# Kernel optimization log

Hardware: AMD Instinct MI355X
Metric: run time of the kernel (lower is better)

Reference implementation:

```python
import jax, jax.numpy as jnp
import numpy as np

N_GRAPHS = 500
CHAIN = 200
D_STATE = 64
HID = 128
NEG_SLOPE = 0.2  # PyG GATConv default


def setup_inputs() -> dict:
    key = jax.random.key(0)
    ks = jax.random.split(key, 9)
    N = N_GRAPHS * CHAIN
    # batched bidirectional chain graphs (as in create_chain_graph_batch)
    off = np.arange(N_GRAPHS, dtype=np.int32) * CHAIN
    a = (off[:, None] + np.arange(CHAIN - 1, dtype=np.int32)[None, :]).ravel()
    b = a + 1
    edge_index = jnp.asarray(np.stack([np.concatenate([a, b]), np.concatenate([b, a])]), dtype=jnp.int32)
    x = jax.random.normal(ks[0], (N, D_STATE), jnp.float32)
    s1 = 1.0 / np.sqrt(D_STATE)
    W1 = jax.random.normal(ks[1], (D_STATE, 2 * HID), jnp.float32) * s1
    att_src1 = jax.random.normal(ks[2], (2, HID), jnp.float32) * (1.0 / np.sqrt(HID))
    att_dst1 = jax.random.normal(ks[3], (2, HID), jnp.float32) * (1.0 / np.sqrt(HID))
    b1 = jnp.zeros((2 * HID,), jnp.float32)
    s2 = 1.0 / np.sqrt(2 * HID)
    W2 = jax.random.normal(ks[4], (2 * HID, HID), jnp.float32) * s2
    att_src2 = jax.random.normal(ks[5], (1, HID), jnp.float32) * (1.0 / np.sqrt(HID))
    att_dst2 = jax.random.normal(ks[6], (1, HID), jnp.float32) * (1.0 / np.sqrt(HID))
    b2 = jnp.zeros((HID,), jnp.float32)
    return {"x": x, "edge_index": edge_index, "W1": W1, "att_src1": att_src1,
            "att_dst1": att_dst1, "b1": b1, "W2": W2, "att_src2": att_src2,
            "att_dst2": att_dst2, "b2": b2}


def gat_conv(x, src, dst, W, att_src, att_dst, bias, concat):
    # PyG GATConv: per-head linear, additive attention, segment softmax over dst
    N = x.shape[0]
    H, C = att_src.shape
    h = (x @ W).reshape(N, H, C)                          # [N,H,C]
    a_s = (h * att_src).sum(-1)                           # [N,H]
    a_d = (h * att_dst).sum(-1)                           # [N,H]
    logits = jax.nn.leaky_relu(a_s[src] + a_d[dst], NEG_SLOPE)  # [E,H]
    m = jax.ops.segment_max(logits, dst, num_segments=N)
    e = jnp.exp(logits - m[dst])
    s = jax.ops.segment_sum(e, dst, num_segments=N)
    alpha = e / (s[dst] + 1e-16)                          # [E,H]
    out = jax.ops.segment_sum(h[src] * alpha[:, :, None], dst, num_segments=N)  # [N,H,C]
    out = out.reshape(N, H * C) if concat else out.mean(axis=1)
    return out + bias


def reference(x, edge_index, W1, att_src1, att_dst1, b1, W2, att_src2, att_dst2, b2):
    N = x.shape[0]
    loop = jnp.arange(N, dtype=edge_index.dtype)
    src = jnp.concatenate([edge_index[0], loop])  # add_self_loops=True (PyG default)
    dst = jnp.concatenate([edge_index[1], loop])
    h = gat_conv(x, src, dst, W1, att_src1, att_dst1, b1, concat=True)
    h = jax.nn.gelu(h, approximate=False)  # torch F.gelu default = exact erf
    h = gat_conv(h, src, dst, W2, att_src2, att_dst2, b2, concat=False)
    return jax.nn.gelu(h, approximate=False)
```

## Files before the change

kernel.cpp:

```cpp
#include <hip/hip_runtime.h>
#include <hip/hip_bf16.h>

#define NG 500
#define CH 200
#define NN (NG*CH)
#define DS 64
#define HDIM 128
#define C1 256
#define NEG_SLOPE 0.2f
#define GB 1563

typedef unsigned short ushort_t;
typedef __attribute__((ext_vector_type(8))) short bf16x8;
typedef __attribute__((ext_vector_type(4))) float f32x4;

__device__ __forceinline__ float us2f(ushort_t u){
  union { unsigned int i; float f; } v; v.i = ((unsigned int)u) << 16; return v.f;
}
__device__ __forceinline__ ushort_t f2us(float f){
  union { float f; unsigned int i; } v; v.f = f;
  unsigned int x = v.i;
  return (ushort_t)((x + 0x7fffu + ((x >> 16) & 1u)) >> 16);
}
__device__ __forceinline__ unsigned int cvt_pk_bf16(float a, float b){
  unsigned int r;
  asm("v_cvt_pk_bf16_f32 %0, %1, %2" : "=v"(r) : "v"(a), "v"(b));
  return r;
}
__device__ __forceinline__ float lrelu(float v){ return v > 0.f ? v : NEG_SLOPE * v; }
__device__ __forceinline__ float gelu_fast(float x){
  float x2 = x * x;
  float zn = x * fmaf(-0.0713548163f, x2, -1.5957691216f);
  float e  = __expf(zn);
  return x * __builtin_amdgcn_rcpf(1.f + e);
}

__global__ void probe_dtype(const void* __restrict__ x, int* __restrict__ flag){
  __shared__ int cnt;
  if (threadIdx.x == 0) cnt = 0;
  __syncthreads();
  const ushort_t* p = (const ushort_t*)x;
  int local = 0;
  for (int i = threadIdx.x; i < 8192; i += 256) {
    float v = us2f(p[i]);
    if (!(fabsf(v) < 100.f)) local++;
  }
  atomicAdd(&cnt, local);
  __syncthreads();
  if (threadIdx.x == 0) flag[0] = (cnt > 16) ? 1 : 0;
}

__global__ void prep_w(const int* __restrict__ flag,
                       const void* W1, const void* as1, const void* ad1, const void* b1,
                       const void* W2, const void* as2, const void* ad2, const void* b2,
                       ushort_t* w1t, ushort_t* w2t,
                       float* asrc1f, float* adst1f, float* b1f,
                       float* asrc2f, float* adst2f, float* b2f,
                       ushort_t* wsd1, ushort_t* wsd2)
{
  const bool F = flag[0] != 0;
  int i = blockIdx.x * 256 + threadIdx.x;
  #define LD(p, j) (F ? ((const float*)(p))[j] : us2f(((const ushort_t*)(p))[j]))
  if (i < 16384)      { int k = i >> 8, n = i & 255; w1t[n*64  + k] = f2us(LD(W1, i)); }
  else if (i < 49152) { int j = i - 16384, k = j >> 7, n = j & 127; w2t[n*256 + k] = f2us(LD(W2, j)); }
  else if (i < 49408) { asrc1f[i-49152] = LD(as1, i-49152); }
  else if (i < 49664) { adst1f[i-49408] = LD(ad1, i-49408); }
  else if (i < 49920) { b1f[i-49664]    = LD(b1,  i-49664); }
  else if (i < 50048) { asrc2f[i-49920] = LD(as2, i-49920); }
  else if (i < 50176) { adst2f[i-50048] = LD(ad2, i-50048); }
  else if (i < 50304) { b2f[i-50176]    = LD(b2,  i-50176); }
  else if (i < 50560) {
    int j = i - 50304, k = j >> 2, c = j & 3;
    int head = c >> 1;
    const void* av = (c & 1) ? ad1 : as1;
    float s = 0.f;
    for (int cc = 0; cc < 128; cc++)
      s += LD(W1, k*256 + head*128 + cc) * LD(av, head*128 + cc);
    ushort_t hi = f2us(s);
    wsd1[c*64 + k] = hi;
    wsd1[(c+4)*64 + k] = f2us(s - us2f(hi));
  }
  else if (i < 51072) {
    int j = i - 50560, k = j >> 1, c = j & 1;
    const void* av = c ? ad2 : as2;
    float s = 0.f;
    for (int cc = 0; cc < 128; cc++)
      s += LD(W2, k*128 + cc) * LD(av, cc);
    ushort_t hi = f2us(s);
    wsd2[c*256 + k] = hi;
    wsd2[(c+2)*256 + k] = f2us(s - us2f(hi));
  }
  else if (i < 51584) { wsd1[512  + (i - 51072)] = 0; }
  else if (i < 54656) { wsd2[1024 + (i - 51584)] = 0; }
  #undef LD
}

__global__ __launch_bounds__(256, 4) void fused(
    const int* __restrict__ flag, const void* __restrict__ x,
    const ushort_t* __restrict__ w1t, const ushort_t* __restrict__ w2t,
    const ushort_t* __restrict__ wsd1, const ushort_t* __restrict__ wsd2,
    const float* __restrict__ b1f, const float* __restrict__ b2f,
    void* __restrict__ out)
{
  __shared__ ushort_t lds[17952];
  __shared__ float scratch[800];
  ushort_t* As  = lds;
  ushort_t* g1L = lds;

  const int t  = threadIdx.x;
  const int m0 = blockIdx.x * 64;
  const int l = t & 63, w = t >> 6;
  const int ln = l & 15, quad = l >> 4;
  const bool F = flag[0] != 0;

  #pragma unroll
  for (int i = 0; i < 5; i++) {
    int q = t + i*256;
    int r = q >> 4, off = (q & 15) * 4;
    int gr = m0 - 2 + r;
    if (r < 68 && gr >= 0 && gr < NN) {
      if (F) {
        float4 xv = *(const float4*)(&((const float*)x)[(size_t)gr*DS + off]);
        uint2 u; u.x = cvt_pk_bf16(xv.x, xv.y); u.y = cvt_pk_bf16(xv.z, xv.w);
        *(uint2*)(&As[r*72 + off]) = u;
      } else {
        *(ushort4*)(&As[r*72 + off]) = *(const ushort4*)(&((const ushort_t*)x)[(size_t)gr*DS + off]);
      }
    } else {
      ushort4 z = {0,0,0,0};
      *(ushort4*)(&As[r*72 + off]) = z;
    }
  }

  f32x4 acc[5][4];
  #pragma unroll
  for (int mi = 0; mi < 5; mi++)
    #pragma unroll
    for (int nj = 0; nj < 4; nj++) acc[mi][nj] = (f32x4){0.f,0.f,0.f,0.f};
  f32x4 acc_att[5];
  #pragma unroll
  for (int mi = 0; mi < 5; mi++) acc_att[mi] = (f32x4){0.f,0.f,0.f,0.f};

  __syncthreads();
  #pragma unroll
  for (int h = 0; h < 2; h++) {
    #pragma unroll
    for (int ks = 0; ks < 2; ks++) {
      const int kk = ks*32 + quad*8;
      bf16x8 a[5], b[2];
      #pragma unroll
      for (int njl = 0; njl < 2; njl++)
        b[njl] = *(const bf16x8*)(&w1t[(w*64 + h*32 + njl*16 + ln)*64 + kk]);
      #pragma unroll
      for (int mi = 0; mi < 5; mi++) a[mi] = *(const bf16x8*)(&As[(mi*16 + ln)*72 + kk]);
      #pragma unroll
      for (int mi = 0; mi < 5; mi++)
        #pragma unroll
        for (int njl = 0; njl < 2; njl++)
          acc[mi][2*h+njl] = __builtin_amdgcn_mfma_f32_16x16x32_bf16(a[mi], b[njl], acc[mi][2*h+njl], 0, 0, 0);
      if (h == 0 && w == 0) {
        bf16x8 batt = *(const bf16x8*)(&wsd1[ln*64 + kk]);
        #pragma unroll
        for (int mi = 0; mi < 5; mi++)
          acc_att[mi] = __builtin_amdgcn_mfma_f32_16x16x32_bf16(a[mi], batt, acc_att[mi], 0, 0, 0);
      }
    }
  }

  if (w == 0) {
    #pragma unroll
    for (int mi = 0; mi < 5; mi++)
      #pragma unroll
      for (int r = 0; r < 4; r++) {
        float v = acc_att[mi][r];
        float vc = v + __shfl(v, (l + 4) & 63, 64);
        int row = mi*16 + quad*4 + r;
        if (ln < 4 && row < 68) scratch[ln*68 + row] = vc;
      }
  }
  __syncthreads();

  if (t < 132) {
    int hh = (t >= 66) ? 1 : 0;
    int n  = t - 66*hh;
    int gj = m0 - 1 + n;
    int p  = gj % CH;
    const float* Sa = &scratch[(2*hh)*68];
    const float* Da = &scratch[(2*hh+1)*68];
    float ad = Da[n+1], as_s = Sa[n+1], as_l = Sa[n], as_r = Sa[n+2];
    bool hl = p > 0, hr = p < CH-1;
    float zs = lrelu(as_s + ad);
    float zl = hl ? lrelu(as_l + ad) : -1e30f;
    float zr = hr ? lrelu(as_r + ad) : -1e30f;
    float mx = fmaxf(zs, fmaxf(zl, zr));
    float el = hl ? __expf(zl - mx) : 0.f;
    float es = __expf(zs - mx);
    float er = hr ? __expf(zr - mx) : 0.f;
    float inv = __builtin_amdgcn_rcpf(el + es + er + 1e-16f);
    scratch[272 + n*8 + hh*4 + 0] = el*inv;
    scratch[272 + n*8 + hh*4 + 1] = es*inv;
    scratch[272 + n*8 + hh*4 + 2] = er*inv;
  }
  __syncthreads();

  {
    float b1v[4];
    #pragma unroll
    for (int nj = 0; nj < 4; nj++) b1v[nj] = b1f[w*64 + nj*16 + ln];
    if (t < 128) {
      int rr = (t < 64) ? 0 : 67;
      int c4 = (t & 63) * 4;
      ushort4 z = {0,0,0,0};
      *(ushort4*)(&g1L[rr*264 + c4]) = z;
    }
    const int head = w >> 1;
    #pragma unroll
    for (int mi = 0; mi < 5; mi++) {
      const int mip = (mi < 4) ? mi+1 : 4;
      const int mim = (mi > 0) ? mi-1 : 0;
      float hp3[4], hm0[4];
      #pragma unroll
      for (int nj = 0; nj < 4; nj++) {
        float up_a = __shfl(acc[mi ][nj][0], (l+16)&63, 64);
        float up_b = __shfl(acc[mip][nj][0], (l+16)&63, 64);
        float dn_a = __shfl(acc[mi ][nj][3], (l-16)&63, 64);
        float dn_b = __shfl(acc[mim][nj][3], (l-16)&63, 64);
        hp3[nj] = (quad < 3) ? up_a : up_b;
        hm0[nj] = (quad > 0) ? dn_a : dn_b;
      }
      #pragma unroll
      for (int r = 0; r < 4; r++) {
        int row = mi*16 + quad*4 + r;
        if (row >= 1 && row <= 66) {
          float4 av = *(const float4*)(&scratch[272 + (row-1)*8 + head*4]);
          float o[4];
          #pragma unroll
          for (int nj = 0; nj < 4; nj++) {
            float self = acc[mi][nj][r];
            float hm = (r > 0) ? acc[mi][nj][r-1] : hm0[nj];
            float hp = (r < 3) ? acc[mi][nj][r+1] : hp3[nj];
            o[nj] = gelu_fast(av.y*self + av.x*hm + av.z*hp + b1v[nj]);
          }
          unsigned int u01 = cvt_pk_bf16(o[0], o[1]);
          unsigned int u23 = cvt_pk_bf16(o[2], o[3]);
          ushort_t* base = &g1L[row*264 + w*64 + ln];
          base[0]  = (ushort_t)u01; base[16] = (ushort_t)(u01 >> 16);
          base[32] = (ushort_t)u23; base[48] = (ushort_t)(u23 >> 16);
        }
      }
    }
  }
  __syncthreads();

  f32x4 acc2[5][2];
  #pragma unroll
  for (int mi = 0; mi < 5; mi++)
    #pragma unroll
    for (int nj = 0; nj < 2; nj++) acc2[mi][nj] = (f32x4){0.f,0.f,0.f,0.f};
  f32x4 acc2_att[5];
  #pragma unroll
  for (int mi = 0; mi < 5; mi++) acc2_att[mi] = (f32x4){0.f,0.f,0.f,0.f};

  #pragma unroll
  for (int ck = 0; ck < 4; ck++) {
    bf16x8 a2[2][5];
    #pragma unroll
    for (int ks = 0; ks < 2; ks++)
      #pragma unroll
      for (int mi = 0; mi < 5; mi++) {
        int ar = mi*16 + ln;
        if (mi == 4) ar = (ar < 67) ? ar : 67;
        a2[ks][mi] = *(const bf16x8*)(&g1L[ar*264 + ck*64 + ks*32 + quad*8]);
      }
    if (ck == w) {
      #pragma unroll
      for (int ks = 0; ks < 2; ks++) {
        bf16x8 batt2 = *(const bf16x8*)(&wsd2[ln*256 + ck*64 + ks*32 + quad*8]);
        #pragma unroll
        for (int mi = 0; mi < 5; mi++)
          acc2_att[mi] = __builtin_amdgcn_mfma_f32_16x16x32_bf16(a2[ks][mi], batt2, acc2_att[mi], 0, 0, 0);
      }
    }
    #pragma unroll
    for (int h2 = 0; h2 < 2; h2++) {
      #pragma unroll
      for (int ks = 0; ks < 2; ks++) {
        bf16x8 b = *(const bf16x8*)(&w2t[(w*32 + h2*16 + ln)*256 + ck*64 + ks*32 + quad*8]);
        #pragma unroll
        for (int mi = 0; mi < 5; mi++)
          acc2[mi][h2] = __builtin_amdgcn_mfma_f32_16x16x32_bf16(a2[ks][mi], b, acc2[mi][h2], 0, 0, 0);
      }
    }
  }

  #pragma unroll
  for (int mi = 0; mi < 5; mi++)
    #pragma unroll
    for (int r = 0; r < 4; r++) {
      float v = acc2_att[mi][r];
      float vc = v + __shfl(v, (l + 2) & 63, 64);
      int row = mi*16 + quad*4 + r;
      if (ln < 2 && row < 68) scratch[(w*2 + ln)*68 + row] = vc;
    }
  __syncthreads();

  if (t < 64) {
    int gi = m0 + t;
    if (gi < NN) {
      int p = gi % CH;
      float ad = 0.f, as_s = 0.f, as_l = 0.f, as_r = 0.f;
      #pragma unroll
      for (int ww = 0; ww < 4; ww++) {
        as_s += scratch[(ww*2)*68 + t+2];
        as_l += scratch[(ww*2)*68 + t+1];
        as_r += scratch[(ww*2)*68 + t+3];
        ad   += scratch[(ww*2+1)*68 + t+2];
      }
      bool hl = p > 0, hr = p < CH-1;
      float zs = lrelu(as_s + ad);
      float zl = hl ? lrelu(as_l + ad) : -1e30f;
      float zr = hr ? lrelu(as_r + ad) : -1e30f;
      float mx = fmaxf(zs, fmaxf(zl, zr));
      float el = hl ? __expf(zl - mx) : 0.f;
      float es = __expf(zs - mx);
      float er = hr ? __expf(zr - mx) : 0.f;
      float inv = __builtin_amdgcn_rcpf(el + es + er + 1e-16f);
      scratch[544 + t*4 + 0] = el*inv;
      scratch[544 + t*4 + 1] = es*inv;
      scratch[544 + t*4 + 2] = er*inv;
    }
  }
  __syncthreads();

  {
    float b2v[2];
    #pragma unroll
    for (int nj = 0; nj < 2; nj++) b2v[nj] = b2f[w*32 + nj*16 + ln];
    #pragma unroll
    for (int mi = 0; mi < 5; mi++) {
      const int mip = (mi < 4) ? mi+1 : 4;
      const int mim = (mi > 0) ? mi-1 : 0;
      float hp3[2], hm0[2];
      #pragma unroll
      for (int nj = 0; nj < 2; nj++) {
        float up_a = __shfl(acc2[mi ][nj][0], (l+16)&63, 64);
        float up_b = __shfl(acc2[mip][nj][0], (l+16)&63, 64);
        float dn_a = __shfl(acc2[mi ][nj][3], (l-16)&63, 64);
        float dn_b = __shfl(acc2[mim][nj][3], (l-16)&63, 64);
        hp3[nj] = (quad < 3) ? up_a : up_b;
        hm0[nj] = (quad > 0) ? dn_a : dn_b;
      }
      #pragma unroll
      for (int r = 0; r < 4; r++) {
        int row = mi*16 + quad*4 + r;
        if (row >= 2 && row <= 65) {
          int n = row - 2;
          int gi = m0 + n;
          if (gi < NN) {
            float4 av = *(const float4*)(&scratch[544 + n*4]);
            float o0, o1;
            {
              float self = acc2[mi][0][r];
              float hm = (r > 0) ? acc2[mi][0][r-1] : hm0[0];
              float hp = (r < 3) ? acc2[mi][0][r+1] : hp3[0];
              o0 = gelu_fast(av.y*self + av.x*hm + av.z*hp + b2v[0]);
            }
            {
              float self = acc2[mi][1][r];
              float hm = (r > 0) ? acc2[mi][1][r-1] : hm0[1];
              float hp = (r < 3) ? acc2[mi][1][r+1] : hp3[1];
              o1 = gelu_fast(av.y*self + av.x*hm + av.z*hp + b2v[1]);
            }
            int c2 = w*32 + ln;
            if (F) {
              ((float*)out)[(size_t)gi*HDIM + c2]      = o0;
              ((float*)out)[(size_t)gi*HDIM + c2 + 16] = o1;
            } else {
              unsigned int u = cvt_pk_bf16(o0, o1);
              ((ushort_t*)out)[(size_t)gi*HDIM + c2]      = (ushort_t)u;
              ((ushort_t*)out)[(size_t)gi*HDIM + c2 + 16] = (ushort_t)(u >> 16);
            }
          }
        }
      }
    }
  }
}

extern "C" void kernel_launch(void* const* d_in, const int* in_sizes, int n_in,
                              void* d_out, int out_size, void* d_ws, size_t ws_size,
                              hipStream_t stream)
{
  const void* x   = d_in[0];
  const void* W1  = d_in[2];
  const void* as1 = d_in[3];
  const void* ad1 = d_in[4];
  const void* b1  = d_in[5];
  const void* W2  = d_in[6];
  const void* as2 = d_in[7];
  const void* ad2 = d_in[8];
  const void* b2  = d_in[9];

  char* w = (char*)d_ws;
  size_t off = 0;
  int* flag = (int*)w;                       off += 256;
  ushort_t* w1t = (ushort_t*)(w + off);      off += 64 * 256 * 2;
  ushort_t* w2t = (ushort_t*)(w + off);      off += 256 * 128 * 2;
  float* asrc1f = (float*)(w + off);         off += 256 * 4;
  float* adst1f = (float*)(w + off);         off += 256 * 4;
  float* b1f    = (float*)(w + off);         off += 256 * 4;
  float* asrc2f = (float*)(w + off);         off += 128 * 4;
  float* adst2f = (float*)(w + off);         off += 128 * 4;
  float* b2f    = (float*)(w + off);         off += 128 * 4;
  ushort_t* wsd1 = (ushort_t*)(w + off);     off += 16 * 64 * 2;
  ushort_t* wsd2 = (ushort_t*)(w + off);     off += 16 * 256 * 2;

  probe_dtype<<<1, 256, 0, stream>>>(x, flag);
  prep_w<<<214, 256, 0, stream>>>(flag, W1, as1, ad1, b1, W2, as2, ad2, b2,
                                  w1t, w2t, asrc1f, adst1f, b1f, asrc2f, adst2f, b2f,
                                  wsd1, wsd2);
  fused<<<GB, 256, 0, stream>>>(flag, x, w1t, w2t, wsd1, wsd2, b1f, b2f, d_out);
}
```

Baseline: 177.9 us.

## Double fused kernel to 512 threads and parallelize attention-weight prep dots

The fused GAT kernel moves from 4 to 8 wavefronts per 64-node block, so each wave computes half as many output columns in both GEMM stages. This lowers per-thread accumulator registers and adds parallelism across the block. The prep kernel now splits each 128-long attention dot product across 16 lanes with shuffle reductions, and drops the unused float copies of the attention vectors. The trade-off is more waves competing for LDS and barriers, and the launch-bounds occupancy hint at 512 threads may constrain registers.

```diff
diff --git a/kernel.cpp b/kernel.cpp
--- a/kernel.cpp
+++ b/kernel.cpp
@@ -54,8 +54,7 @@
                        const void* W1, const void* as1, const void* ad1, const void* b1,
                        const void* W2, const void* as2, const void* ad2, const void* b2,
                        ushort_t* w1t, ushort_t* w2t,
-                       float* asrc1f, float* adst1f, float* b1f,
-                       float* asrc2f, float* adst2f, float* b2f,
+                       float* b1f, float* b2f,
                        ushort_t* wsd1, ushort_t* wsd2)
 {
   const bool F = flag[0] != 0;
@@ -63,39 +62,50 @@
   #define LD(p, j) (F ? ((const float*)(p))[j] : us2f(((const ushort_t*)(p))[j]))
   if (i < 16384)      { int k = i >> 8, n = i & 255; w1t[n*64  + k] = f2us(LD(W1, i)); }
   else if (i < 49152) { int j = i - 16384, k = j >> 7, n = j & 127; w2t[n*256 + k] = f2us(LD(W2, j)); }
-  else if (i < 49408) { asrc1f[i-49152] = LD(as1, i-49152); }
-  else if (i < 49664) { adst1f[i-49408] = LD(ad1, i-49408); }
-  else if (i < 49920) { b1f[i-49664]    = LD(b1,  i-49664); }
-  else if (i < 50048) { asrc2f[i-49920] = LD(as2, i-49920); }
-  else if (i < 50176) { adst2f[i-50048] = LD(ad2, i-50048); }
-  else if (i < 50304) { b2f[i-50176]    = LD(b2,  i-50176); }
-  else if (i < 50560) {
-    int j = i - 50304, k = j >> 2, c = j & 3;
-    int head = c >> 1;
+  else if (i < 49408) { b1f[i-49152] = LD(b1, i-49152); }
+  else if (i < 49536) { b2f[i-49408] = LD(b2, i-49408); }
+  else if (i < 53632) {
+    int j = i - 49536, dot = j >> 4, lsub = j & 15;
+    int k = dot >> 2, c = dot & 3, head = c >> 1;
     const void* av = (c & 1) ? ad1 : as1;
     float s = 0.f;
-    for (int cc = 0; cc < 128; cc++)
+    #pragma unroll
+    for (int jj = 0; jj < 8; jj++) {
+      int cc = lsub*8 + jj;
       s += LD(W1, k*256 + head*128 + cc) * LD(av, head*128 + cc);
-    ushort_t hi = f2us(s);
-    wsd1[c*64 + k] = hi;
-    wsd1[(c+4)*64 + k] = f2us(s - us2f(hi));
-  }
-  else if (i < 51072) {
-    int j = i - 50560, k = j >> 1, c = j & 1;
+    }
+    s += __shfl_xor(s, 1, 64); s += __shfl_xor(s, 2, 64);
+    s += __shfl_xor(s, 4, 64); s += __shfl_xor(s, 8, 64);
+    if (lsub == 0) {
+      ushort_t hi = f2us(s);
+      wsd1[c*64 + k] = hi;
+      wsd1[(c+4)*64 + k] = f2us(s - us2f(hi));
+    }
+  }
+  else if (i < 61824) {
+    int j = i - 53632, dot = j >> 4, lsub = j & 15;
+    int k = dot >> 1, c = dot & 1;
     const void* av = c ? ad2 : as2;
     float s = 0.f;
-    for (int cc = 0; cc < 128; cc++)
+    #pragma unroll
+    for (int jj = 0; jj < 8; jj++) {
+      int cc = lsub*8 + jj;
       s += LD(W2, k*128 + cc) * LD(av, cc);
-    ushort_t hi = f2us(s);
-    wsd2[c*256 + k] = hi;
-    wsd2[(c+2)*256 + k] = f2us(s - us2f(hi));
-  }
-  else if (i < 51584) { wsd1[512  + (i - 51072)] = 0; }
-  else if (i < 54656) { wsd2[1024 + (i - 51584)] = 0; }
+    }
+    s += __shfl_xor(s, 1, 64); s += __shfl_xor(s, 2, 64);
+    s += __shfl_xor(s, 4, 64); s += __shfl_xor(s, 8, 64);
+    if (lsub == 0) {
+      ushort_t hi = f2us(s);
+      wsd2[c*256 + k] = hi;
+      wsd2[(c+2)*256 + k] = f2us(s - us2f(hi));
+    }
+  }
+  else if (i < 62336) { wsd1[512  + (i - 61824)] = 0; }
+  else if (i < 65408) { wsd2[1024 + (i - 62336)] = 0; }
   #undef LD
 }
 
-__global__ __launch_bounds__(256, 4) void fused(
+__global__ __launch_bounds__(512, 4) void fused(
     const int* __restrict__ flag, const void* __restrict__ x,
     const ushort_t* __restrict__ w1t, const ushort_t* __restrict__ w2t,
     const ushort_t* __restrict__ wsd1, const ushort_t* __restrict__ wsd2,
@@ -114,8 +124,9 @@
   const bool F = flag[0] != 0;
 
   #pragma unroll
-  for (int i = 0; i < 5; i++) {
-    int q = t + i*256;
+  for (int i = 0; i < 3; i++) {
+    int q = t + i*512;
+    if (q >= 1280) break;
     int r = q >> 4, off = (q & 15) * 4;
     int gr = m0 - 2 + r;
     if (r < 68 && gr >= 0 && gr < NN) {
@@ -132,38 +143,35 @@
     }
   }
 
-  f32x4 acc[5][4];
+  f32x4 acc[5][2];
   #pragma unroll
   for (int mi = 0; mi < 5; mi++)
     #pragma unroll
-    for (int nj = 0; nj < 4; nj++) acc[mi][nj] = (f32x4){0.f,0.f,0.f,0.f};
+    for (int nj = 0; nj < 2; nj++) acc[mi][nj] = (f32x4){0.f,0.f,0.f,0.f};
   f32x4 acc_att[5];
   #pragma unroll
   for (int mi = 0; mi < 5; mi++) acc_att[mi] = (f32x4){0.f,0.f,0.f,0.f};
 
   __syncthreads();
   #pragma unroll
-  for (int h = 0; h < 2; h++) {
-    #pragma unroll
-    for (int ks = 0; ks < 2; ks++) {
-      const int kk = ks*32 + quad*8;
-      bf16x8 a[5], b[2];
-      #pragma unroll
-      for (int njl = 0; njl < 2; njl++)
-        b[njl] = *(const bf16x8*)(&w1t[(w*64 + h*32 + njl*16 + ln)*64 + kk]);
-      #pragma unroll
-      for (int mi = 0; mi < 5; mi++) a[mi] = *(const bf16x8*)(&As[(mi*16 + ln)*72 + kk]);
+  for (int ks = 0; ks < 2; ks++) {
+    const int kk = ks*32 + quad*8;
+    bf16x8 a[5], b[2];
+    #pragma unroll
+    for (int nj = 0; nj < 2; nj++)
+      b[nj] = *(const bf16x8*)(&w1t[(w*32 + nj*16 + ln)*64 + kk]);
+    #pragma unroll
+    for (int mi = 0; mi < 5; mi++) a[mi] = *(const bf16x8*)(&As[(mi*16 + ln)*72 + kk]);
+    #pragma unroll
+    for (int mi = 0; mi < 5; mi++)
+      #pragma unroll
+      for (int nj = 0; nj < 2; nj++)
+        acc[mi][nj] = __builtin_amdgcn_mfma_f32_16x16x32_bf16(a[mi], b[nj], acc[mi][nj], 0, 0, 0);
+    if (w == 0) {
+      bf16x8 batt = *(const bf16x8*)(&wsd1[ln*64 + kk]);
       #pragma unroll
       for (int mi = 0; mi < 5; mi++)
-        #pragma unroll
-        for (int njl = 0; njl < 2; njl++)
-          acc[mi][2*h+njl] = __builtin_amdgcn_mfma_f32_16x16x32_bf16(a[mi], b[njl], acc[mi][2*h+njl], 0, 0, 0);
-      if (h == 0 && w == 0) {
-        bf16x8 batt = *(const bf16x8*)(&wsd1[ln*64 + kk]);
-        #pragma unroll
-        for (int mi = 0; mi < 5; mi++)
-          acc_att[mi] = __builtin_amdgcn_mfma_f32_16x16x32_bf16(a[mi], batt, acc_att[mi], 0, 0, 0);
-      }
+        acc_att[mi] = __builtin_amdgcn_mfma_f32_16x16x32_bf16(a[mi], batt, acc_att[mi], 0, 0, 0);
     }
   }
 
@@ -204,23 +212,23 @@
   __syncthreads();
 
   {
-    float b1v[4];
-    #pragma unroll
-    for (int nj = 0; nj < 4; nj++) b1v[nj] = b1f[w*64 + nj*16 + ln];
+    float b1v[2];
+    #pragma unroll
+    for (int nj = 0; nj < 2; nj++) b1v[nj] = b1f[w*32 + nj*16 + ln];
     if (t < 128) {
       int rr = (t < 64) ? 0 : 67;
       int c4 = (t & 63) * 4;
       ushort4 z = {0,0,0,0};
       *(ushort4*)(&g1L[rr*264 + c4]) = z;
     }
-    const int head = w >> 1;
+    const int head = w >> 2;
     #pragma unroll
     for (int mi = 0; mi < 5; mi++) {
       const int mip = (mi < 4) ? mi+1 : 4;
       const int mim = (mi > 0) ? mi-1 : 0;
-      float hp3[4], hm0[4];
-      #pragma unroll
-      for (int nj = 0; nj < 4; nj++) {
+      float hp3[2], hm0[2];
+      #pragma unroll
+      for (int nj = 0; nj < 2; nj++) {
         float up_a = __shfl(acc[mi ][nj][0], (l+16)&63, 64);
         float up_b = __shfl(acc[mip][nj][0], (l+16)&63, 64);
         float dn_a = __shfl(acc[mi ][nj][3], (l-16)&63, 64);
@@ -233,75 +241,67 @@
         int row = mi*16 + quad*4 + r;
         if (row >= 1 && row <= 66) {
           float4 av = *(const float4*)(&scratch[272 + (row-1)*8 + head*4]);
-          float o[4];
+          float o[2];
           #pragma unroll
-          for (int nj = 0; nj < 4; nj++) {
+          for (int nj = 0; nj < 2; nj++) {
             float self = acc[mi][nj][r];
             float hm = (r > 0) ? acc[mi][nj][r-1] : hm0[nj];
             float hp = (r < 3) ? acc[mi][nj][r+1] : hp3[nj];
             o[nj] = gelu_fast(av.y*self + av.x*hm + av.z*hp + b1v[nj]);
           }
           unsigned int u01 = cvt_pk_bf16(o[0], o[1]);
-          unsigned int u23 = cvt_pk_bf16(o[2], o[3]);
-          ushort_t* base = &g1L[row*264 + w*64 + ln];
-          base[0]  = (ushort_t)u01; base[16] = (ushort_t)(u01 >> 16);
-          base[32] = (ushort_t)u23; base[48] = (ushort_t)(u23 >> 16);
+          ushort_t* base = &g1L[row*264 + w*32 + ln];
+          base[0]  = (ushort_t)u01;
+          base[16] = (ushort_t)(u01 >> 16);
         }
       }
     }
   }
   __syncthreads();
 
-  f32x4 acc2[5][2];
-  #pragma unroll
-  for (int mi = 0; mi < 5; mi++)
-    #pragma unroll
-    for (int nj = 0; nj < 2; nj++) acc2[mi][nj] = (f32x4){0.f,0.f,0.f,0.f};
+  f32x4 acc2[5];
+  #pragma unroll
+  for (int mi = 0; mi < 5; mi++) acc2[mi] = (f32x4){0.f,0.f,0.f,0.f};
   f32x4 acc2_att[5];
   #pragma unroll
   for (int mi = 0; mi < 5; mi++) acc2_att[mi] = (f32x4){0.f,0.f,0.f,0.f};
 
   #pragma unroll
   for (int ck = 0; ck < 4; ck++) {
-    bf16x8 a2[2][5];
-    #pragma unroll
-    for (int ks = 0; ks < 2; ks++)
+    #pragma unroll
+    for (int ks = 0; ks < 2; ks++) {
+      const int kk = ks*32 + quad*8;
+      bf16x8 a2[5];
       #pragma unroll
       for (int mi = 0; mi < 5; mi++) {
         int ar = mi*16 + ln;
         if (mi == 4) ar = (ar < 67) ? ar : 67;
-        a2[ks][mi] = *(const bf16x8*)(&g1L[ar*264 + ck*64 + ks*32 + quad*8]);
-      }
-    if (ck == w) {
-      #pragma unroll
-      for (int ks = 0; ks < 2; ks++) {
-        bf16x8 batt2 = *(const bf16x8*)(&wsd2[ln*256 + ck*64 + ks*32 + quad*8]);
+        a2[mi] = *(const bf16x8*)(&g1L[ar*264 + ck*64 + kk]);
+      }
+      bf16x8 b = *(const bf16x8*)(&w2t[(w*16 + ln)*256 + ck*64 + kk]);
+      #pragma unroll
+      for (int mi = 0; mi < 5; mi++)
+        acc2[mi] = __builtin_amdgcn_mfma_f32_16x16x32_bf16(a2[mi], b, acc2[mi], 0, 0, 0);
+      if (w == ck) {
+        bf16x8 batt2 = *(const bf16x8*)(&wsd2[ln*256 + ck*64 + kk]);
         #pragma unroll
         for (int mi = 0; mi < 5; mi++)
-          acc2_att[mi] = __builtin_amdgcn_mfma_f32_16x16x32_bf16(a2[ks][mi], batt2, acc2_att[mi], 0, 0, 0);
-      }
-    }
-    #pragma unroll
-    for (int h2 = 0; h2 < 2; h2++) {
-      #pragma unroll
-      for (int ks = 0; ks < 2; ks++) {
-        bf16x8 b = *(const bf16x8*)(&w2t[(w*32 + h2*16 + ln)*256 + ck*64 + ks*32 + quad*8]);
-        #pragma unroll
-        for (int mi = 0; mi < 5; mi++)
-          acc2[mi][h2] = __builtin_amdgcn_mfma_f32_16x16x32_bf16(a2[ks][mi], b, acc2[mi][h2], 0, 0, 0);
-      }
-    }
-  }
-
-  #pragma unroll
-  for (int mi = 0; mi < 5; mi++)
-    #pragma unroll
-    for (int r = 0; r < 4; r++) {
-      float v = acc2_att[mi][r];
-      float vc = v + __shfl(v, (l + 2) & 63, 64);
-      int row = mi*16 + quad*4 + r;
-      if (ln < 2 && row < 68) scratch[(w*2 + ln)*68 + row] = vc;
-    }
+          acc2_att[mi] = __builtin_amdgcn_mfma_f32_16x16x32_bf16(a2[mi], batt2, acc2_att[mi], 0, 0, 0);
+      }
+    }
+  }
+
+  if (w < 4) {
+    #pragma unroll
+    for (int mi = 0; mi < 5; mi++)
+      #pragma unroll
+      for (int r = 0; r < 4; r++) {
+        float v = acc2_att[mi][r];
+        float vc = v + __shfl(v, (l + 2) & 63, 64);
+        int row = mi*16 + quad*4 + r;
+        if (ln < 2 && row < 68) scratch[(w*2 + ln)*68 + row] = vc;
+      }
+  }
   __syncthreads();
 
   if (t < 64) {
@@ -333,22 +333,19 @@
   __syncthreads();
 
   {
-    float b2v[2];
-    #pragma unroll
-    for (int nj = 0; nj < 2; nj++) b2v[nj] = b2f[w*32 + nj*16 + ln];
+    float b2v = b2f[w*16 + ln];
     #pragma unroll
     for (int mi = 0; mi < 5; mi++) {
       const int mip = (mi < 4) ? mi+1 : 4;
       const int mim = (mi > 0) ? mi-1 : 0;
-      float hp3[2], hm0[2];
-      #pragma unroll
-      for (int nj = 0; nj < 2; nj++) {
-        float up_a = __shfl(acc2[mi ][nj][0], (l+16)&63, 64);
-        float up_b = __shfl(acc2[mip][nj][0], (l+16)&63, 64);
-        float dn_a = __shfl(acc2[mi ][nj][3], (l-16)&63, 64);
-        float dn_b = __shfl(acc2[mim][nj][3], (l-16)&63, 64);
-        hp3[nj] = (quad < 3) ? up_a : up_b;
-        hm0[nj] = (quad > 0) ? dn_a : dn_b;
+      float hp3, hm0;
+      {
+        float up_a = __shfl(acc2[mi ][0], (l+16)&63, 64);
+        float up_b = __shfl(acc2[mip][0], (l+16)&63, 64);
+        float dn_a = __shfl(acc2[mi ][3], (l-16)&63, 64);
+        float dn_b = __shfl(acc2[mim][3], (l-16)&63, 64);
+        hp3 = (quad < 3) ? up_a : up_b;
+        hm0 = (quad > 0) ? dn_a : dn_b;
       }
       #pragma unroll
       for (int r = 0; r < 4; r++) {
@@ -358,28 +355,13 @@
           int gi = m0 + n;
           if (gi < NN) {
             float4 av = *(const float4*)(&scratch[544 + n*4]);
-            float o0, o1;
-            {
-              float self = acc2[mi][0][r];
-              float hm = (r > 0) ? acc2[mi][0][r-1] : hm0[0];
-              float hp = (r < 3) ? acc2[mi][0][r+1] : hp3[0];
-              o0 = gelu_fast(av.y*self + av.x*hm + av.z*hp + b2v[0]);
-            }
-            {
-              float self = acc2[mi][1][r];
-              float hm = (r > 0) ? acc2[mi][1][r-1] : hm0[1];
-              float hp = (r < 3) ? acc2[mi][1][r+1] : hp3[1];
-              o1 = gelu_fast(av.y*self + av.x*hm + av.z*hp + b2v[1]);
-            }
-            int c2 = w*32 + ln;
-            if (F) {
-              ((float*)out)[(size_t)gi*HDIM + c2]      = o0;
-              ((float*)out)[(size_t)gi*HDIM + c2 + 16] = o1;
-            } else {
-              unsigned int u = cvt_pk_bf16(o0, o1);
-              ((ushort_t*)out)[(size_t)gi*HDIM + c2]      = (ushort_t)u;
-              ((ushort_t*)out)[(size_t)gi*HDIM + c2 + 16] = (ushort_t)(u >> 16);
-            }
+            float self = acc2[mi][r];
+            float hm = (r > 0) ? acc2[mi][r-1] : hm0;
+            float hp = (r < 3) ? acc2[mi][r+1] : hp3;
+            float o = gelu_fast(av.y*self + av.x*hm + av.z*hp + b2v);
+            int c2 = w*16 + ln;
+            if (F) ((float*)out)[(size_t)gi*HDIM + c2] = o;
+            else   ((ushort_t*)out)[(size_t)gi*HDIM + c2] = f2us(o);
           }
         }
       }
@@ -406,18 +388,13 @@
   int* flag = (int*)w;                       off += 256;
   ushort_t* w1t = (ushort_t*)(w + off);      off += 64 * 256 * 2;
   ushort_t* w2t = (ushort_t*)(w + off);      off += 256 * 128 * 2;
-  float* asrc1f = (float*)(w + off);         off += 256 * 4;
-  float* adst1f = (float*)(w + off);         off += 256 * 4;
   float* b1f    = (float*)(w + off);         off += 256 * 4;
-  float* asrc2f = (float*)(w + off);         off += 128 * 4;
-  float* adst2f = (float*)(w + off);         off += 128 * 4;
   float* b2f    = (float*)(w + off);         off += 128 * 4;
   ushort_t* wsd1 = (ushort_t*)(w + off);     off += 16 * 64 * 2;
   ushort_t* wsd2 = (ushort_t*)(w + off);     off += 16 * 256 * 2;
 
   probe_dtype<<<1, 256, 0, stream>>>(x, flag);
-  prep_w<<<214, 256, 0, stream>>>(flag, W1, as1, ad1, b1, W2, as2, ad2, b2,
-                                  w1t, w2t, asrc1f, adst1f, b1f, asrc2f, adst2f, b2f,
-                                  wsd1, wsd2);
-  fused<<<GB, 256, 0, stream>>>(flag, x, w1t, w2t, wsd1, wsd2, b1f, b2f, d_out);
-}
+  prep_w<<<256, 256, 0, stream>>>(flag, W1, as1, ad1, b1, W2, as2, ad2, b2,
+                                  w1t, w2t, b1f, b2f, wsd1, wsd2);
+  fused<<<GB, 512, 0, stream>>>(flag, x, w1t, w2t, wsd1, wsd2, b1f, b2f, d_out);
+}
```

New measurement: 158.9 us. -10.7%, faster.
